# Kernel tuning notes

Hardware: AMD Instinct MI355X
Metric: run time of the kernel (lower is better)

Reference implementation:

```python
import jax, jax.numpy as jnp
import numpy as np

B, S, H, T = 64, 512, 768, 400


def setup_inputs() -> dict:
    key = jax.random.key(0)
    k1, k2 = jax.random.split(key)
    hidden = jax.random.normal(k1, (B, S, H), dtype=jnp.float32)
    # word_ids: non-decreasing piece->word map per sample, like HF tokenizer word_ids()
    word_ids = jnp.sort(jax.random.randint(k2, (B, S), 0, T), axis=-1).astype(jnp.int32)
    return {"hidden": hidden, "word_ids": word_ids, "num_tokens": T}


def reference(hidden, word_ids, num_tokens):
    # Ragged segment mean-pool: pool subword pieces into per-word reps.
    # hidden: [B, S, H] float; word_ids: [B, S] int in [0, num_tokens)
    b, s, h = hidden.shape
    # Flatten (sample, word) into one global segment id: sample*T + word
    seg = (jnp.arange(b, dtype=word_ids.dtype)[:, None] * num_tokens + word_ids).reshape(-1)
    sums = jax.ops.segment_sum(hidden.reshape(b * s, h), seg, num_segments=b * num_tokens)
    counts = jax.ops.segment_sum(jnp.ones((b * s,), hidden.dtype), seg, num_segments=b * num_tokens)
    # Words with zero pieces -> sum 0 / 1 = 0, matching torch.zeros fallback
    pooled = sums / jnp.maximum(counts, 1.0)[:, None]
    return pooled.reshape(b, num_tokens, h)
```

## Files before the change

kernel.cpp:

```cpp
#include <hip/hip_runtime.h>


#define BB 64
#define SS 512
#define HH 768
#define TT 400
#define H4 (HH / 4)

typedef float f32x4 __attribute__((ext_vector_type(4)));

__global__ __launch_bounds__(256) void build_table_kernel(
    const int* __restrict__ word_ids,
    int* __restrict__ table)
{
    __shared__ int wid[SS];
    __shared__ int sstart[TT];
    __shared__ int send[TT];

    const int b   = blockIdx.x;
    const int tid = threadIdx.x;

    if (tid < SS / 4) {
        reinterpret_cast<int4*>(wid)[tid] =
            reinterpret_cast<const int4*>(word_ids + b * SS)[tid];
    }
    for (int t = tid; t < TT; t += 256) { sstart[t] = 0; send[t] = 0; }
    __syncthreads();

    for (int s = tid; s < SS; s += 256) {
        const int w = wid[s];
        if (s == 0      || wid[s - 1] != w) sstart[w] = s;
        if (s == SS - 1 || wid[s + 1] != w) send[w]   = s + 1;
    }
    __syncthreads();

    for (int t = tid; t < TT; t += 256) {
        const int st  = sstart[t];
        const int cnt = send[t] - st;
        table[b * TT + t] = st | (cnt << 16);
    }
}

__global__ __launch_bounds__(256) void pool_kernel(
    const float* __restrict__ hidden,
    const int* __restrict__ table,
    float* __restrict__ out)
{
    const int wave = threadIdx.x >> 6;
    const int lane = threadIdx.x & 63;
    const int bt   = blockIdx.x * 4 + wave;
    const int b    = bt / TT;

    const int pack  = table[bt];
    const int start = pack & 0xFFFF;
    const int cnt   = pack >> 16;

    const f32x4* hrow = reinterpret_cast<const f32x4*>(hidden)
                        + ((size_t)b * SS + start) * H4;
    f32x4* orow = reinterpret_cast<f32x4*>(out) + (size_t)bt * H4;

    f32x4 a0 = {0.f, 0.f, 0.f, 0.f};
    f32x4 a1 = {0.f, 0.f, 0.f, 0.f};
    f32x4 a2 = {0.f, 0.f, 0.f, 0.f};

    for (int i = 0; i < cnt; ++i) {
        const f32x4* p = hrow + (size_t)i * H4;
        a0 += p[lane];
        a1 += p[lane + 64];
        a2 += p[lane + 128];
    }

    const float inv = (cnt > 1) ? (1.0f / (float)cnt) : 1.0f;
    a0 *= inv; a1 *= inv; a2 *= inv;

    __builtin_nontemporal_store(a0, &orow[lane]);
    __builtin_nontemporal_store(a1, &orow[lane + 64]);
    __builtin_nontemporal_store(a2, &orow[lane + 128]);
}

extern "C" void kernel_launch(void* const* d_in, const int* in_sizes, int n_in,
                              void* d_out, int out_size, void* d_ws, size_t ws_size,
                              hipStream_t stream) {
    (void)in_sizes; (void)n_in; (void)ws_size; (void)out_size;
    const float* hidden   = (const float*)d_in[0];
    const int*   word_ids = (const int*)d_in[1];
    float*       out      = (float*)d_out;
    int*         table    = (int*)d_ws;

    build_table_kernel<<<dim3(BB), dim3(256), 0, stream>>>(word_ids, table);
    pool_kernel<<<dim3(BB * TT / 4), dim3(256), 0, stream>>>(hidden, table, out);
}
```

Baseline: 177.6 us.

## Process eight words per wave with speculative paired row loads

Each wave now handles eight consecutive words instead of one. It fetches their table entries with a single load and broadcasts them via readlane. For each pair of words it issues the first and last hidden-row loads up front, unconditionally, and masks them by count, so that several independent loads are in flight before the inner loop for longer segments runs. This aims to hide memory latency on the short, data-dependent segments. The cost is fewer blocks, more registers, and redundant loads for empty or single-piece words.

```diff
diff --git a/kernel.cpp b/kernel.cpp
--- a/kernel.cpp
+++ b/kernel.cpp
@@ -6,6 +6,9 @@
 #define HH 768
 #define TT 400
 #define H4 (HH / 4)
+#define RPW 8
+#define WPB 4
+#define NBLK (BB * TT / (WPB * RPW))
 
 typedef float f32x4 __attribute__((ext_vector_type(4)));
 
@@ -46,36 +49,74 @@
     const int* __restrict__ table,
     float* __restrict__ out)
 {
-    const int wave = threadIdx.x >> 6;
-    const int lane = threadIdx.x & 63;
-    const int bt   = blockIdx.x * 4 + wave;
-    const int b    = bt / TT;
+    const int wave    = threadIdx.x >> 6;
+    const int lane    = threadIdx.x & 63;
+    const int base_bt = (blockIdx.x * WPB + wave) * RPW;
+    const int b       = base_bt / TT;
 
-    const int pack  = table[bt];
-    const int start = pack & 0xFFFF;
-    const int cnt   = pack >> 16;
+    const int mypack = table[base_bt + (lane & (RPW - 1))];
 
-    const f32x4* hrow = reinterpret_cast<const f32x4*>(hidden)
-                        + ((size_t)b * SS + start) * H4;
-    f32x4* orow = reinterpret_cast<f32x4*>(out) + (size_t)bt * H4;
+    const f32x4* hb = reinterpret_cast<const f32x4*>(hidden) + (size_t)b * SS * H4;
+    f32x4*       ob = reinterpret_cast<f32x4*>(out) + (size_t)base_bt * H4;
 
-    f32x4 a0 = {0.f, 0.f, 0.f, 0.f};
-    f32x4 a1 = {0.f, 0.f, 0.f, 0.f};
-    f32x4 a2 = {0.f, 0.f, 0.f, 0.f};
+    #pragma unroll
+    for (int j = 0; j < RPW; j += 2) {
+        const int p0 = __builtin_amdgcn_readlane(mypack, j);
+        const int p1 = __builtin_amdgcn_readlane(mypack, j + 1);
+        const int s0 = p0 & 0xFFFF, c0 = p0 >> 16;
+        const int s1 = p1 & 0xFFFF, c1 = p1 >> 16;
+        const int e0 = s0 + ((c0 > 1) ? (c0 - 1) : 0);
+        const int e1 = s1 + ((c1 > 1) ? (c1 - 1) : 0);
 
-    for (int i = 0; i < cnt; ++i) {
-        const f32x4* p = hrow + (size_t)i * H4;
-        a0 += p[lane];
-        a1 += p[lane + 64];
-        a2 += p[lane + 128];
+        const f32x4* r0a = hb + (size_t)s0 * H4;
+        const f32x4* r0b = hb + (size_t)e0 * H4;
+        const f32x4* r1a = hb + (size_t)s1 * H4;
+        const f32x4* r1b = hb + (size_t)e1 * H4;
+
+        f32x4 va0 = r0a[lane], va1 = r0a[lane + 64], va2 = r0a[lane + 128];
+        f32x4 vb0 = r0b[lane], vb1 = r0b[lane + 64], vb2 = r0b[lane + 128];
+        f32x4 wa0 = r1a[lane], wa1 = r1a[lane + 64], wa2 = r1a[lane + 128];
+        f32x4 wb0 = r1b[lane], wb1 = r1b[lane + 64], wb2 = r1b[lane + 128];
+
+        const float ka = (c0 >= 1) ? 1.f : 0.f;
+        const float kb = (c0 >= 2) ? 1.f : 0.f;
+        const float la = (c1 >= 1) ? 1.f : 0.f;
+        const float lb = (c1 >= 2) ? 1.f : 0.f;
+
+        f32x4 A0 = va0 * ka + vb0 * kb;
+        f32x4 A1 = va1 * ka + vb1 * kb;
+        f32x4 A2 = va2 * ka + vb2 * kb;
+        f32x4 B0 = wa0 * la + wb0 * lb;
+        f32x4 B1 = wa1 * la + wb1 * lb;
+        f32x4 B2 = wa2 * la + wb2 * lb;
+
+        if (c0 > 2) {
+            const f32x4* p = hb + (size_t)(s0 + 1) * H4;
+            for (int i = 0; i < c0 - 2; ++i, p += H4) {
+                A0 += p[lane]; A1 += p[lane + 64]; A2 += p[lane + 128];
+            }
+        }
+        if (c1 > 2) {
+            const f32x4* p = hb + (size_t)(s1 + 1) * H4;
+            for (int i = 0; i < c1 - 2; ++i, p += H4) {
+                B0 += p[lane]; B1 += p[lane + 64]; B2 += p[lane + 128];
+            }
+        }
+
+        const float i0 = 1.f / (float)((c0 > 1) ? c0 : 1);
+        const float i1 = 1.f / (float)((c1 > 1) ? c1 : 1);
+        A0 *= i0; A1 *= i0; A2 *= i0;
+        B0 *= i1; B1 *= i1; B2 *= i1;
+
+        f32x4* o0 = ob + (size_t)j * H4;
+        f32x4* o1 = ob + (size_t)(j + 1) * H4;
+        __builtin_nontemporal_store(A0, &o0[lane]);
+        __builtin_nontemporal_store(A1, &o0[lane + 64]);
+        __builtin_nontemporal_store(A2, &o0[lane + 128]);
+        __builtin_nontemporal_store(B0, &o1[lane]);
+        __builtin_nontemporal_store(B1, &o1[lane + 64]);
+        __builtin_nontemporal_store(B2, &o1[lane + 128]);
     }
-
-    const float inv = (cnt > 1) ? (1.0f / (float)cnt) : 1.0f;
-    a0 *= inv; a1 *= inv; a2 *= inv;
-
-    __builtin_nontemporal_store(a0, &orow[lane]);
-    __builtin_nontemporal_store(a1, &orow[lane + 64]);
-    __builtin_nontemporal_store(a2, &orow[lane + 128]);
 }
 
 extern "C" void kernel_launch(void* const* d_in, const int* in_sizes, int n_in,
@@ -88,5 +129,5 @@
     int*         table    = (int*)d_ws;
 
     build_table_kernel<<<dim3(BB), dim3(256), 0, stream>>>(word_ids, table);
-    pool_kernel<<<dim3(BB * TT / 4), dim3(256), 0, stream>>>(hidden, table, out);
+    pool_kernel<<<dim3(NBLK), dim3(256), 0, stream>>>(hidden, table, out);
 }
```

After: 186.4 us. +5.0%, slower.
